# Performance work log

Measured on AMD Instinct MI355X. Metric: run time of the kernel, lower is better.

## Reference

```python
import jax, jax.numpy as jnp
import numpy as np

IMAGE_SIZE = 1024
DOWNSIZING = 64
THRESHOLD = 0.65  # default_threshold_target (threshold arg == 0)
NUM_BG_POINTS = 1
ORI_SHAPE = (2160, 3840)
EMBED_C, FEAT_H, FEAT_W = 256, 64, 64


def setup_inputs() -> dict:
    key = jax.random.key(0)
    k1, k2 = jax.random.split(key)
    image_embeddings = jax.random.normal(k1, (1, EMBED_C, FEAT_H, FEAT_W), dtype=jnp.float32)
    reference_feat = jax.random.normal(k2, (1, EMBED_C), dtype=jnp.float32) * 0.1
    ori_shape = jnp.array(ORI_SHAPE, dtype=jnp.int32)
    return {"image_embeddings": image_embeddings, "reference_feat": reference_feat, "ori_shape": ori_shape}


def _postprocess_masks(sim, H, W):
    # F.interpolate to (image_size, image_size), crop to pre-padded size, resize to ori_shape
    sim = jax.image.resize(sim, (1, 1, IMAGE_SIZE, IMAGE_SIZE), method="bilinear", antialias=False)
    scale = IMAGE_SIZE / max(H, W)
    ph = int(np.floor(H * scale + 0.5))
    pw = int(np.floor(W * scale + 0.5))
    sim = sim[..., :ph, :pw]
    return jax.image.resize(sim, (1, 1, H, W), method="bilinear", antialias=False)


def reference(image_embeddings, reference_feat, ori_shape):
    H, W = int(ori_shape[0]), int(ori_shape[1])
    # --- similarity map ---
    t = image_embeddings[0]                                   # (C, hf, wf)
    c, hf, wf = t.shape
    t = t / jnp.linalg.norm(t, axis=0, keepdims=True)         # channel-wise L2 norm
    sim = (reference_feat @ t.reshape(c, hf * wf)).reshape(1, 1, hf, wf)
    sim = _postprocess_masks(sim, H, W)
    m = sim[0, 0]                                             # (H, W)
    flat = m.reshape(-1)                                      # (H*W,)
    hw = H * W

    # --- background points: k smallest values ---
    _, bg_idx = jax.lax.top_k(-flat, NUM_BG_POINTS)
    bg_row = bg_idx // W
    bg_col = bg_idx % W
    bg_coords = jnp.stack([bg_col, bg_row], axis=1).astype(jnp.float32)  # (N, 2) = (x, y)

    # --- foreground points: grid-binned per-cell max (segment-max form of
    #     torch.where + unique + broadcast-equality + per-bin topk) ---
    ratio = IMAGE_SIZE / max(H, W)
    n_cells_side = IMAGE_SIZE // DOWNSIZING                    # 16; bounds grid rows/cols
    num_cells = n_cells_side * n_cells_side                    # 256 fixed
    idx = jnp.arange(hw, dtype=jnp.int32)
    ys = idx // W
    xs = idx % W
    gy = jnp.floor(ys * (ratio / DOWNSIZING)).astype(jnp.int32)
    gx = jnp.floor(xs * (ratio / DOWNSIZING)).astype(jnp.int32)
    seg = gy * n_cells_side + gx                               # grid id per pixel

    valid = flat > THRESHOLD
    masked = jnp.where(valid, flat, -jnp.inf)
    seg_max = jax.ops.segment_max(masked, seg, num_segments=num_cells)
    # first pixel achieving the cell max (matches torch.topk tie behavior)
    is_max = valid & (masked == seg_max[seg])
    cand = jnp.where(is_max, idx, hw)
    best = jax.ops.segment_min(cand, seg, num_segments=num_cells)
    cell_valid = best < hw
    bi = jnp.minimum(best, hw - 1)
    px = (bi % W).astype(jnp.float32)
    py = (bi // W).astype(jnp.float32)
    ps = flat[bi]
    points = jnp.stack([px, py, ps], axis=1)                   # (num_cells, 3) = (x, y, score)
    points = jnp.where(cell_valid[:, None], points, -1.0)      # mimic F.pad(value=-1) rows
    sort_key = jnp.where(cell_valid, ps, -jnp.inf)
    order = jnp.argsort(-sort_key)                             # score descending, invalid last
    points_scores = points[order]
    return points_scores, bg_coords
```

## Files before the change

kernel.cpp:

```cpp
#include <hip/hip_runtime.h>

#define W_OUT 3840
#define H_OUT 2160
#define IW 1024
#define IH 576

__device__ __forceinline__ unsigned int enc_f32(float f) {
    unsigned int b = __float_as_uint(f);
    return (b & 0x80000000u) ? ~b : (b | 0x80000000u);
}

__global__ __launch_bounds__(256) void sim_kernel(
    const float* __restrict__ emb, const float* __restrict__ ref,
    float* __restrict__ sim, unsigned long long* __restrict__ cells,
    unsigned long long* __restrict__ bg)
{
    const int lane = threadIdx.x & 63;
    const int wave = threadIdx.x >> 6;
    const int p = blockIdx.x * 64 + lane;
    const int cbase = wave * 64;
    float dot = 0.f, ss = 0.f;
#pragma unroll 8
    for (int cc = 0; cc < 64; ++cc) {
        int c = cbase + cc;
        float a = emb[c * 4096 + p];
        dot = fmaf(ref[c], a, dot);
        ss  = fmaf(a, a, ss);
    }
    __shared__ float sdot[4][64];
    __shared__ float sss[4][64];
    sdot[wave][lane] = dot;
    sss[wave][lane]  = ss;
    __syncthreads();
    if (wave == 0) {
        float d = (sdot[0][lane] + sdot[1][lane]) + (sdot[2][lane] + sdot[3][lane]);
        float s = (sss[0][lane] + sss[1][lane]) + (sss[2][lane] + sss[3][lane]);
        sim[p] = d / sqrtf(s);
    }
    if (blockIdx.x == 0) {
        cells[threadIdx.x] = 0ull;
        if (threadIdx.x == 0) *bg = 0xFFFFFFFFFFFFFFFFull;
    }
}

__global__ __launch_bounds__(256) void scan_kernel(
    const float* __restrict__ sim,
    unsigned long long* __restrict__ cells,
    unsigned long long* __restrict__ bg)
{
    __shared__ float ldsI[2][IW];
    __shared__ unsigned long long red[256];

    const float INV375 = (float)(1.0 / 3.75);
    const float INV16  = 0.0625f;
    const float CELL_R = (float)(1024.0 / 3840.0 / 64.0);

    const int y   = blockIdx.x;
    const int tid = threadIdx.x;

    float fy  = ((float)y + 0.5f) * INV375 - 0.5f;
    float fyf = floorf(fy);
    float wy  = fy - fyf;
    int ai = (int)fyf;
    int a1 = min(max(ai + 1, 0), IH - 1);
    int a0 = min(max(ai,     0), IH - 1);

    for (int r = 0; r < 2; ++r) {
        int a = (r == 0) ? a0 : a1;
        float fa  = ((float)a + 0.5f) * INV16 - 0.5f;
        float faf = floorf(fa);
        float wa  = fa - faf;
        int si = (int)faf;
        int s1 = min(max(si + 1, 0), 63);
        int s0 = min(max(si,     0), 63);
        const float* row0 = sim + s0 * 64;
        const float* row1 = sim + s1 * 64;
        for (int b = tid; b < IW; b += 256) {
            float fb  = ((float)b + 0.5f) * INV16 - 0.5f;
            float fbf = floorf(fb);
            float wb  = fb - fbf;
            int ci = (int)fbf;
            int c1 = min(max(ci + 1, 0), 63);
            int c0 = min(max(ci,     0), 63);
            float v0 = row0[c0] * (1.f - wb) + row0[c1] * wb;
            float v1 = row1[c0] * (1.f - wb) + row1[c1] * wb;
            ldsI[r][b] = v0 * (1.f - wa) + v1 * wa;
        }
    }
    __syncthreads();

    unsigned long long best = 0xFFFFFFFFFFFFFFFFull;
#pragma unroll
    for (int k = 0; k < 15; ++k) {
        int x = k * 256 + tid;
        float fx  = ((float)x + 0.5f) * INV375 - 0.5f;
        float fxf = floorf(fx);
        float wx  = fx - fxf;
        int bi = (int)fxf;
        int b1 = min(max(bi + 1, 0), IW - 1);
        int b0 = min(max(bi,     0), IW - 1);
        float v0 = ldsI[0][b0] * (1.f - wx) + ldsI[0][b1] * wx;
        float v1 = ldsI[1][b0] * (1.f - wx) + ldsI[1][b1] * wx;
        float F  = v0 * (1.f - wy) + v1 * wy;

        unsigned int idx = (unsigned int)(y * W_OUT + x);
        unsigned long long key = ((unsigned long long)enc_f32(F) << 32) | (unsigned long long)idx;
        if (key < best) best = key;

        if (F > 0.65f) {
            int gx = (int)floorf((float)x * CELL_R);
            int gy = (int)floorf((float)y * CELL_R);
            int seg = gy * 16 + gx;
            unsigned long long ck =
                ((unsigned long long)__float_as_uint(F) << 32) |
                (unsigned long long)(0xFFFFFFFFu - idx);
            atomicMax(&cells[seg], ck);
        }
    }

    red[tid] = best;
    __syncthreads();
    for (int s = 128; s > 0; s >>= 1) {
        if (tid < s) {
            unsigned long long o = red[tid + s];
            if (o < red[tid]) red[tid] = o;
        }
        __syncthreads();
    }
    if (tid == 0) atomicMin(bg, red[0]);
}

__global__ __launch_bounds__(256) void finalize_kernel(
    const unsigned long long* __restrict__ cells,
    const unsigned long long* __restrict__ bg,
    float* __restrict__ out)
{
    __shared__ float sk[256];
    const int t = threadIdx.x;
    unsigned long long ck = cells[t];
    float px = -1.f, py = -1.f, ps = -1.f;
    float key = -__builtin_huge_valf();
    if (ck != 0ull) {
        unsigned int bits = (unsigned int)(ck >> 32);
        unsigned int idx  = 0xFFFFFFFFu - (unsigned int)(ck & 0xFFFFFFFFull);
        float v = __uint_as_float(bits);
        px = (float)(idx % W_OUT);
        py = (float)(idx / W_OUT);
        ps = v;
        key = v;
    }
    sk[t] = key;
    __syncthreads();
    int rank = 0;
    for (int j = 0; j < 256; ++j) {
        float kj = sk[j];
        if (kj > key || (kj == key && j < t)) rank++;
    }
    out[rank * 3 + 0] = px;
    out[rank * 3 + 1] = py;
    out[rank * 3 + 2] = ps;
    if (t == 0) {
        unsigned long long b = *bg;
        unsigned int idx = (unsigned int)(b & 0xFFFFFFFFull);
        out[256 * 3 + 0] = (float)(idx % W_OUT);
        out[256 * 3 + 1] = (float)(idx / W_OUT);
    }
}

extern "C" void kernel_launch(void* const* d_in, const int* in_sizes, int n_in,
                              void* d_out, int out_size, void* d_ws, size_t ws_size,
                              hipStream_t stream) {
    (void)in_sizes; (void)n_in; (void)out_size; (void)ws_size;
    const float* emb = (const float*)d_in[0];
    const float* ref = (const float*)d_in[1];
    float* out = (float*)d_out;

    float* sim = (float*)d_ws;
    unsigned long long* cells = (unsigned long long*)((char*)d_ws + 4096*4);
    unsigned long long* bg    = cells + 256;

    sim_kernel<<<64, 256, 0, stream>>>(emb, ref, sim, cells, bg);
    scan_kernel<<<H_OUT, 256, 0, stream>>>(sim, cells, bg);
    finalize_kernel<<<1, 256, 0, stream>>>(cells, bg, out);
}
```

Baseline: 100.9 us.

## Assign contiguous pixel runs per thread with register stencils and wave-shuffle reductions

Each thread now handles 15 contiguous output pixels instead of a strided set. The needed row samples are loaded once as float4 registers, and the column indices are hard-coded per pixel. Per-pixel threshold atomics are replaced by an unconditional per-thread cell max, a 16-lane shuffle reduction, and one atomicMax per cell per row. The LDS tree reduction for the background minimum becomes wave shuffles. The threshold test moves to finalize by decoding the order-preserving key. Edge threads keep the generic path, and correctness relies on the hard-coded index table matching the 3.75 scale.

```diff
diff --git a/kernel.cpp b/kernel.cpp
--- a/kernel.cpp
+++ b/kernel.cpp
@@ -7,7 +7,7 @@
 
 __device__ __forceinline__ unsigned int enc_f32(float f) {
     unsigned int b = __float_as_uint(f);
-    return (b & 0x80000000u) ? ~b : (b | 0x80000000u);
+    return b ^ (0x80000000u | (unsigned int)((int)b >> 31));
 }
 
 __global__ __launch_bounds__(256) void sim_kernel(
@@ -48,12 +48,12 @@
     unsigned long long* __restrict__ cells,
     unsigned long long* __restrict__ bg)
 {
-    __shared__ float ldsI[2][IW];
-    __shared__ unsigned long long red[256];
+    __shared__ float4 I4[2][IW / 4];
+    float* I0 = (float*)&I4[0][0];
+    float* I1 = (float*)&I4[1][0];
 
     const float INV375 = (float)(1.0 / 3.75);
     const float INV16  = 0.0625f;
-    const float CELL_R = (float)(1024.0 / 3840.0 / 64.0);
 
     const int y   = blockIdx.x;
     const int tid = threadIdx.x;
@@ -75,6 +75,7 @@
         int s0 = min(max(si,     0), 63);
         const float* row0 = sim + s0 * 64;
         const float* row1 = sim + s1 * 64;
+        float* dst = (r == 0) ? I0 : I1;
         for (int b = tid; b < IW; b += 256) {
             float fb  = ((float)b + 0.5f) * INV16 - 0.5f;
             float fbf = floorf(fb);
@@ -84,50 +85,78 @@
             int c0 = min(max(ci,     0), 63);
             float v0 = row0[c0] * (1.f - wb) + row0[c1] * wb;
             float v1 = row1[c0] * (1.f - wb) + row1[c1] * wb;
-            ldsI[r][b] = v0 * (1.f - wa) + v1 * wa;
+            dst[b] = v0 * (1.f - wa) + v1 * wa;
         }
     }
     __syncthreads();
 
-    unsigned long long best = 0xFFFFFFFFFFFFFFFFull;
+    unsigned long long bestCell = 0ull;
+    unsigned long long bestBg   = 0xFFFFFFFFFFFFFFFFull;
+    const int x0 = tid * 15;
+    const unsigned int idxBase = (unsigned int)(y * W_OUT + x0);
+
+#define UPD(F, jj) {                                                        \
+        unsigned long long top = ((unsigned long long)enc_f32(F)) << 32;    \
+        unsigned int idx = idxBase + (jj);                                  \
+        unsigned long long bgk = top | (unsigned long long)idx;             \
+        unsigned long long ck  = top | (unsigned long long)(~idx);          \
+        if (ck  > bestCell) bestCell = ck;                                  \
+        if (bgk < bestBg)   bestBg   = bgk;                                 \
+    }
+
+    if (tid == 0 || tid == 255) {
 #pragma unroll
-    for (int k = 0; k < 15; ++k) {
-        int x = k * 256 + tid;
-        float fx  = ((float)x + 0.5f) * INV375 - 0.5f;
-        float fxf = floorf(fx);
-        float wx  = fx - fxf;
-        int bi = (int)fxf;
-        int b1 = min(max(bi + 1, 0), IW - 1);
-        int b0 = min(max(bi,     0), IW - 1);
-        float v0 = ldsI[0][b0] * (1.f - wx) + ldsI[0][b1] * wx;
-        float v1 = ldsI[1][b0] * (1.f - wx) + ldsI[1][b1] * wx;
-        float F  = v0 * (1.f - wy) + v1 * wy;
-
-        unsigned int idx = (unsigned int)(y * W_OUT + x);
-        unsigned long long key = ((unsigned long long)enc_f32(F) << 32) | (unsigned long long)idx;
-        if (key < best) best = key;
-
-        if (F > 0.65f) {
-            int gx = (int)floorf((float)x * CELL_R);
-            int gy = (int)floorf((float)y * CELL_R);
-            int seg = gy * 16 + gx;
-            unsigned long long ck =
-                ((unsigned long long)__float_as_uint(F) << 32) |
-                (unsigned long long)(0xFFFFFFFFu - idx);
-            atomicMax(&cells[seg], ck);
+        for (int j = 0; j < 15; ++j) {
+            int x = x0 + j;
+            float fx  = ((float)x + 0.5f) * INV375 - 0.5f;
+            float fxf = floorf(fx);
+            float wx  = fx - fxf;
+            int bi = (int)fxf;
+            int b1 = min(max(bi + 1, 0), IW - 1);
+            int b0 = min(max(bi,     0), IW - 1);
+            float v0 = I0[b0] * (1.f - wx) + I0[b1] * wx;
+            float v1 = I1[b0] * (1.f - wx) + I1[b1] * wx;
+            float F  = v0 * (1.f - wy) + v1 * wy;
+            UPD(F, j)
         }
-    }
-
-    red[tid] = best;
-    __syncthreads();
-    for (int s = 128; s > 0; s >>= 1) {
-        if (tid < s) {
-            unsigned long long o = red[tid + s];
-            if (o < red[tid]) red[tid] = o;
+    } else {
+        float4 A0 = I4[0][tid - 1], B0 = I4[0][tid], C0 = I4[0][tid + 1];
+        float4 A1 = I4[1][tid - 1], B1 = I4[1][tid], C1 = I4[1][tid + 1];
+        const float rr0[12] = {A0.x,A0.y,A0.z,A0.w, B0.x,B0.y,B0.z,B0.w, C0.x,C0.y,C0.z,C0.w};
+        const float rr1[12] = {A1.x,A1.y,A1.z,A1.w, B1.x,B1.y,B1.z,B1.w, C1.x,C1.y,C1.z,C1.w};
+
+#define PX(j, i0) {                                                         \
+            float fx  = ((float)(x0 + (j)) + 0.5f) * INV375 - 0.5f;         \
+            float fxf = floorf(fx);                                         \
+            float wx  = fx - fxf;                                           \
+            float v0 = rr0[(i0)] * (1.f - wx) + rr0[(i0) + 1] * wx;         \
+            float v1 = rr1[(i0)] * (1.f - wx) + rr1[(i0) + 1] * wx;         \
+            float F  = v0 * (1.f - wy) + v1 * wy;                           \
+            UPD(F, j)                                                       \
         }
-        __syncthreads();
-    }
-    if (tid == 0) atomicMin(bg, red[0]);
+        PX(0,3)  PX(1,3)  PX(2,4)  PX(3,4)  PX(4,4)
+        PX(5,4)  PX(6,5)  PX(7,5)  PX(8,5)  PX(9,6)
+        PX(10,6) PX(11,6) PX(12,6) PX(13,7) PX(14,7)
+#undef PX
+    }
+#undef UPD
+
+#pragma unroll
+    for (int m = 1; m <= 8; m <<= 1) {
+        unsigned long long o = __shfl_xor(bestCell, m, 64);
+        if (o > bestCell) bestCell = o;
+    }
+    if ((tid & 15) == 0) {
+        int seg = (y / 240) * 16 + (tid >> 4);
+        atomicMax(&cells[seg], bestCell);
+    }
+
+#pragma unroll
+    for (int m = 1; m <= 32; m <<= 1) {
+        unsigned long long o = __shfl_xor(bestBg, m, 64);
+        if (o < bestBg) bestBg = o;
+    }
+    if ((tid & 63) == 0) atomicMin(bg, bestBg);
 }
 
 __global__ __launch_bounds__(256) void finalize_kernel(
@@ -140,10 +169,11 @@
     unsigned long long ck = cells[t];
     float px = -1.f, py = -1.f, ps = -1.f;
     float key = -__builtin_huge_valf();
-    if (ck != 0ull) {
-        unsigned int bits = (unsigned int)(ck >> 32);
-        unsigned int idx  = 0xFFFFFFFFu - (unsigned int)(ck & 0xFFFFFFFFull);
-        float v = __uint_as_float(bits);
+    unsigned int e = (unsigned int)(ck >> 32);
+    unsigned int b = (e & 0x80000000u) ? (e ^ 0x80000000u) : ~e;
+    float v = __uint_as_float(b);
+    if (v > 0.65f) {
+        unsigned int idx = ~((unsigned int)(ck & 0xFFFFFFFFull));
         px = (float)(idx % W_OUT);
         py = (float)(idx / W_OUT);
         ps = v;
@@ -160,8 +190,8 @@
     out[rank * 3 + 1] = py;
     out[rank * 3 + 2] = ps;
     if (t == 0) {
-        unsigned long long b = *bg;
-        unsigned int idx = (unsigned int)(b & 0xFFFFFFFFull);
+        unsigned long long bk = *bg;
+        unsigned int idx = (unsigned int)(bk & 0xFFFFFFFFull);
         out[256 * 3 + 0] = (float)(idx % W_OUT);
         out[256 * 3 + 1] = (float)(idx / W_OUT);
     }
```

After: 174.0 us. 72.5% more time.
